# Optimization experiments

Measured on AMD Instinct MI355X. Metric: run time of the kernel, lower is better.

The kernel has to match this reference:

```python
import jax, jax.numpy as jnp
import numpy as np

B, S = 2, 1024            # 2 packed sequences, equal length (offsets = [0, 1024, 2048])
HID, H = 2560, 32
D = HID // H              # 80
ROT = int(0.4 * D)        # 32 partial rotary dims
THETA = 10000.0
MAX_POS = 2048
CACHE_SLOTS = 4096


def setup_inputs() -> dict:
    key = jax.random.key(0)
    ks = jax.random.split(key, 8)
    T = B * S
    w = lambda k: jax.random.normal(k, (HID, HID), dtype=jnp.float32) * 0.02
    return {
        "h": jax.random.normal(ks[0], (T, HID), dtype=jnp.float32),
        "k_cache": jnp.zeros((CACHE_SLOTS, HID), dtype=jnp.float32),
        "v_cache": jnp.zeros((CACHE_SLOTS, HID), dtype=jnp.float32),
        "q_w": w(ks[1]), "q_b": jnp.zeros((HID,), jnp.float32),
        "k_w": w(ks[2]), "k_b": jnp.zeros((HID,), jnp.float32),
        "v_w": w(ks[3]), "v_b": jnp.zeros((HID,), jnp.float32),
        "dense_w": w(ks[4]), "dense_b": jnp.zeros((HID,), jnp.float32),
        "positions": jnp.tile(jnp.arange(S, dtype=jnp.int32), B),
        "offsets": jnp.array([0, S, 2 * S], dtype=jnp.int32),
        "cache_indices": jnp.arange(T, dtype=jnp.int32),
    }


def _rope_tables():
    # neox-style partial rotary tables, [MAX_POS, ROT//2]
    inv_freq = 1.0 / (THETA ** (jnp.arange(0, ROT, 2, dtype=jnp.float32) / ROT))
    freqs = jnp.arange(MAX_POS, dtype=jnp.float32)[:, None] * inv_freq[None, :]
    return jnp.cos(freqs), jnp.sin(freqs)


def _apply_rope(x, cos, sin):
    # x: [T, H, D]; cos/sin: [T, ROT//2] -> rotate first ROT dims, pass rest
    c = cos[:, None, :]
    s = sin[:, None, :]
    x1, x2, rest = x[..., : ROT // 2], x[..., ROT // 2 : ROT], x[..., ROT:]
    return jnp.concatenate([x1 * c - x2 * s, x2 * c + x1 * s, rest], axis=-1)


def reference(h, k_cache, v_cache, q_w, q_b, k_w, k_b, v_w, v_b,
              dense_w, dense_b, positions, offsets, cache_indices):
    T = h.shape[0]
    q = h @ q_w + q_b
    k = h @ k_w + k_b
    v = h @ v_w + v_b

    cos_t, sin_t = _rope_tables()
    cos = cos_t[positions]
    sin = sin_t[positions]
    q = _apply_rope(q.reshape(T, H, D), cos, sin)
    k = _apply_rope(k.reshape(T, H, D), cos, sin)
    v = v.reshape(T, H, D)

    # prompt_init path: scatter freshly-rotated K/V into the flat cache
    k_cache = k_cache.at[cache_indices].set(k.reshape(T, HID))
    v_cache = v_cache.at[cache_indices].set(v.reshape(T, HID))

    # packed_attention: causal attention within each (equal-length) sequence
    q4 = q.reshape(B, S, H, D)
    k4 = k.reshape(B, S, H, D)
    v4 = v.reshape(B, S, H, D)
    scale = D ** -0.5
    scores = jnp.einsum("bqhd,bkhd->bhqk", q4, k4) * scale
    causal = jnp.tril(jnp.ones((S, S), dtype=bool))
    scores = jnp.where(causal[None, None], scores, jnp.float32(-1e9))
    p = jax.nn.softmax(scores, axis=-1)
    o = jnp.einsum("bhqk,bkhd->bqhd", p, v4).reshape(T, HID)

    return o @ dense_w + dense_b
```

## Files before the change

kernel.cpp:

```cpp
#include <hip/hip_runtime.h>
#include <hip/hip_bf16.h>

#define Bq 2
#define Sq 1024
#define Tq 2048
#define HIDq 2560
#define Hq 32
#define Dq 80
#define NQKV 7680

typedef __bf16 bf16x8 __attribute__((ext_vector_type(8)));
typedef float f32x4 __attribute__((ext_vector_type(4)));
typedef unsigned short u16x8 __attribute__((ext_vector_type(8)));
using bf16 = __hip_bfloat16;

__device__ __forceinline__ void gload_lds16(const bf16* g, bf16* l) {
  __builtin_amdgcn_global_load_lds((const __attribute__((address_space(1))) void*)g,
                                   (__attribute__((address_space(3))) void*)l,
                                   16, 0, 0);
}

__global__ __launch_bounds__(256) void cast_h_kernel(const float* __restrict__ h,
                                                     bf16* __restrict__ hb) {
  int i = (blockIdx.x * 256 + threadIdx.x) * 4;
  float4 v = *(const float4*)(h + i);
  bf16 tmp[4];
  tmp[0] = __float2bfloat16(v.x);
  tmp[1] = __float2bfloat16(v.y);
  tmp[2] = __float2bfloat16(v.z);
  tmp[3] = __float2bfloat16(v.w);
  *(ushort4*)(hb + i) = *(ushort4*)tmp;
}

__global__ __launch_bounds__(256) void bias_concat_kernel(const float* __restrict__ qb,
                                                          const float* __restrict__ kb,
                                                          const float* __restrict__ vb,
                                                          float* __restrict__ bqkv) {
  int i = blockIdx.x * 256 + threadIdx.x;
  if (i < HIDq) bqkv[i] = qb[i];
  else if (i < 2 * HIDq) bqkv[i] = kb[i - HIDq];
  else bqkv[i] = vb[i - 2 * HIDq];
}

__global__ __launch_bounds__(256) void wtrans_kernel(const float* __restrict__ qw,
                                                     const float* __restrict__ kw,
                                                     const float* __restrict__ vw,
                                                     const float* __restrict__ dw,
                                                     bf16* __restrict__ wqkvt,
                                                     bf16* __restrict__ wdt) {
  __shared__ float tile[32][33];
  const int z = blockIdx.z;
  const float* src = (z == 0) ? qw : (z == 1) ? kw : (z == 2) ? vw : dw;
  const int n0 = blockIdx.x * 32;
  const int k0 = blockIdx.y * 32;
  const int tx = threadIdx.x, ty = threadIdx.y;
#pragma unroll
  for (int r = 0; r < 4; r++)
    tile[ty + 8 * r][tx] = src[(size_t)(k0 + ty + 8 * r) * HIDq + n0 + tx];
  __syncthreads();
  bf16* dst = (z < 3) ? (wqkvt + (size_t)z * HIDq * HIDq) : wdt;
#pragma unroll
  for (int r = 0; r < 4; r++)
    dst[(size_t)(n0 + ty + 8 * r) * HIDq + k0 + tx] = __float2bfloat16(tile[tx][ty + 8 * r]);
}

__global__ __launch_bounds__(512, 2) void gemm9s_kernel(const bf16* __restrict__ A,
                                                        const bf16* __restrict__ Bt,
                                                        const float* __restrict__ bias,
                                                        bf16* __restrict__ Cout,
                                                        int N, int K, int tM) {
  __shared__ char smem[9 * 16384];
  const int tid = threadIdx.x;
  const int lane = tid & 63;
  const int ln = lane & 15, lg = lane >> 4;
  const int wave = tid >> 6;
  const int wm = wave >> 2;
  const int wn = wave & 3;

  int bid = blockIdx.x, nwg = gridDim.x, swz = bid;
  if ((nwg & 7) == 0) { int cpx = nwg >> 3; swz = (bid & 7) * cpx + (bid >> 3); }
  const int m0 = (swz % tM) * 256;
  const int n0 = (swz / tM) * 256;
  const int NT = K >> 6;

  f32x4 acc[8][4];
  const f32x4 zz = {0.f, 0.f, 0.f, 0.f};
#pragma unroll
  for (int i = 0; i < 8; ++i)
#pragma unroll
    for (int j = 0; j < 4; ++j) acc[i][j] = zz;

  int srow[2], skel[2];
#pragma unroll
  for (int c = 0; c < 2; ++c) {
    const unsigned L = (unsigned)(c * 8192 + tid * 16);
    const unsigned P = L ^ (((L >> 9) & 1u) << 5);
    srow[c] = (int)(P >> 7);
    skel[c] = (int)((P & 127u) >> 1);
  }
  const int wbase = wave * 1024;

  auto STAGE = [&](int H, int ss) {
    const int hh = H & 3;
    const int th = H >> 2;
    const bf16* mat = (hh < 2) ? A : Bt;
    const int rowbase = (hh < 2) ? (m0 + hh * 128) : (n0 + (hh - 2) * 128);
    char* dst = smem + (ss << 14);
#pragma unroll
    for (int c = 0; c < 2; ++c)
      gload_lds16(mat + (size_t)(rowbase + srow[c]) * K + th * 64 + skel[c],
                  (bf16*)(dst + c * 8192 + wbase));
  };

  unsigned offA[2][4][2];
  int     halfA[2][4];
#pragma unroll
  for (int mh = 0; mh < 2; ++mh)
#pragma unroll
    for (int i = 0; i < 4; ++i) {
      const int row = wm * 128 + mh * 64 + i * 16 + ln;
      halfA[mh][i] = row >> 7;
      const int r = row & 127;
#pragma unroll
      for (int kh = 0; kh < 2; ++kh) {
        const unsigned P = (unsigned)(r * 128 + kh * 64 + lg * 16);
        offA[mh][i][kh] = P ^ (((P >> 9) & 1u) << 5);
      }
    }
  unsigned offB[4][2];
  int     halfB[4];
#pragma unroll
  for (int j = 0; j < 4; ++j) {
    const int row = wn * 64 + j * 16 + ln;
    halfB[j] = row >> 7;
    const int r = row & 127;
#pragma unroll
    for (int kh = 0; kh < 2; ++kh) {
      const unsigned P = (unsigned)(r * 128 + kh * 64 + lg * 16);
      offB[j][kh] = P ^ (((P >> 9) & 1u) << 5);
    }
  }

#pragma unroll
  for (int H = 0; H < 5; ++H) STAGE(H, H);

  int s0 = 0;
  for (int t = 0; t < NT; ++t) {
    if (t + 1 < NT) asm volatile("s_waitcnt vmcnt(2)" ::: "memory");
    else            asm volatile("s_waitcnt vmcnt(0)" ::: "memory");
    __builtin_amdgcn_s_barrier();

    int slt[4];
#pragma unroll
    for (int h = 0; h < 4; ++h) { int s = s0 + h; if (s >= 9) s -= 9; slt[h] = s << 14; }

#pragma unroll
    for (int kh = 0; kh < 2; ++kh) {
      bf16x8 bfr[4];
#pragma unroll
      for (int j = 0; j < 4; ++j)
        bfr[j] = *(const bf16x8*)(smem + slt[2 + halfB[j]] + offB[j][kh]);
#pragma unroll
      for (int mh = 0; mh < 2; ++mh) {
        {
          const int p = kh * 2 + mh;
          const int H = 4 * t + p + 5;
          if (H < 4 * NT) {
            int s = s0 + p + 5; if (s >= 9) s -= 9;
            STAGE(H, s);
          }
        }
        bf16x8 af[4];
#pragma unroll
        for (int i = 0; i < 4; ++i)
          af[i] = *(const bf16x8*)(smem + slt[halfA[mh][i]] + offA[mh][i][kh]);
        __builtin_amdgcn_s_setprio(1);
#pragma unroll
        for (int i = 0; i < 4; ++i)
#pragma unroll
          for (int j = 0; j < 4; ++j)
            acc[mh * 4 + i][j] =
                __builtin_amdgcn_mfma_f32_16x16x32_bf16(af[i], bfr[j], acc[mh * 4 + i][j], 0, 0, 0);
        __builtin_amdgcn_s_setprio(0);
      }
    }

    s0 += 4; if (s0 >= 9) s0 -= 9;
  }

#pragma unroll
  for (int i = 0; i < 8; ++i) {
    const int rowb = m0 + wm * 128 + i * 16 + lg * 4;
#pragma unroll
    for (int r = 0; r < 4; ++r) {
#pragma unroll
      for (int j = 0; j < 4; ++j) {
        const int col = n0 + wn * 64 + j * 16 + ln;
        Cout[(size_t)(rowb + r) * N + col] = __float2bfloat16(acc[i][j][r] + bias[col]);
      }
    }
  }
}

template <int MFRAG, int NFRAG, bool OUT_BF16>
__global__ __launch_bounds__(512, 4) void gemm256_kernel(const bf16* __restrict__ A,
                                                         const bf16* __restrict__ Bt,
                                                         const float* __restrict__ bias,
                                                         void* __restrict__ Cout,
                                                         int N, int K, int tMc) {
  constexpr int ACALLS = MFRAG / 4;
  constexpr int BCALLS = NFRAG / 2;
  constexpr int APANEL = 8192 * ACALLS;
  constexpr int BUFSZ = APANEL + 8192 * BCALLS;
  __shared__ char smem[3 * BUFSZ];
  const int tid = threadIdx.x;
  const int lane = tid & 63;
  const int ln = lane & 15, lg = lane >> 4;
  const int wave = tid >> 6;
  const int wm = wave >> 2;
  const int wn = wave & 3;

  int bid = blockIdx.x;
  int swz = bid;
  int nwg = gridDim.x;
  if ((nwg & 7) == 0) { int cpx = nwg >> 3; swz = (bid & 7) * cpx + (bid >> 3); }
  const int m0 = (swz % tMc) * (32 * MFRAG);
  const int n0 = (swz / tMc) * (64 * NFRAG);

  const int NT = K >> 5;

  f32x4 acc[MFRAG][NFRAG];
  const f32x4 zz = {0.f, 0.f, 0.f, 0.f};
#pragma unroll
  for (int i = 0; i < MFRAG; ++i)
#pragma unroll
    for (int j = 0; j < NFRAG; ++j) acc[i][j] = zz;

  const int Rl0 = tid >> 2;
  const int slot = tid & 3;
  const int wbase = (tid >> 6) * 1024;

  auto STAGE = [&](int t, int b) {
    const int k0 = t << 5;
    char* Ab = smem + b * BUFSZ;
    char* Bb = Ab + APANEL;
#pragma unroll
    for (int c = 0; c < ACALLS; ++c) {
      const int srow = c * 128 + Rl0;
      const int row = srow ^ ((srow >> 2) & 1);
      const int col8 = slot ^ (row & 3);
      gload_lds16(A + (size_t)(m0 + row) * K + k0 + col8 * 8,
                  (bf16*)(Ab + c * 8192 + wbase));
    }
#pragma unroll
    for (int c = 0; c < BCALLS; ++c) {
      const int srow = c * 128 + Rl0;
      const int row = srow ^ ((srow >> 2) & 1);
      const int col8 = slot ^ (row & 3);
      gload_lds16(Bt + (size_t)(n0 + row) * K + k0 + col8 * 8,
                  (bf16*)(Bb + c * 8192 + wbase));
    }
  };

  auto FRAG = [&](const char* base, int row) -> bf16x8 {
    const unsigned off = ((unsigned)((row ^ ((row >> 2) & 1)) << 6)) |
                         (((unsigned)lg << 4) ^ ((unsigned)(row & 3) << 4));
    return *(const bf16x8*)(base + off);
  };

  auto WAIT_COUNTED = [&]() {
    constexpr int NCALLS = ACALLS + BCALLS;
    if constexpr (NCALLS == 2)      asm volatile("s_waitcnt vmcnt(2)" ::: "memory");
    else if constexpr (NCALLS == 3) asm volatile("s_waitcnt vmcnt(3)" ::: "memory");
    else                            asm volatile("s_waitcnt vmcnt(4)" ::: "memory");
  };

  STAGE(0, 0);
  STAGE(1, 1);
  WAIT_COUNTED();
  __builtin_amdgcn_s_barrier();

  for (int t = 0; t < NT; ++t) {
    const int cb = t % 3;
    const char* Ab = smem + cb * BUFSZ;
    const char* Bb = Ab + APANEL;
    if (t + 2 < NT) STAGE(t + 2, (t + 2) % 3);

    bf16x8 bfr[NFRAG];
#pragma unroll
    for (int j = 0; j < NFRAG; ++j) bfr[j] = FRAG(Bb, wn * (16 * NFRAG) + j * 16 + ln);
#pragma unroll
    for (int ph = 0; ph < ACALLS; ++ph) {
      bf16x8 af[4];
#pragma unroll
      for (int i = 0; i < 4; ++i)
        af[i] = FRAG(Ab, wm * (16 * MFRAG) + (ph * 4 + i) * 16 + ln);
      __builtin_amdgcn_s_setprio(1);
#pragma unroll
      for (int i = 0; i < 4; ++i)
#pragma unroll
        for (int j = 0; j < NFRAG; ++j)
          acc[ph * 4 + i][j] =
              __builtin_amdgcn_mfma_f32_16x16x32_bf16(af[i], bfr[j], acc[ph * 4 + i][j], 0, 0, 0);
      __builtin_amdgcn_s_setprio(0);
    }

    if (t + 2 < NT) WAIT_COUNTED();
    else            asm volatile("s_waitcnt vmcnt(0)" ::: "memory");
    __builtin_amdgcn_s_barrier();
  }

#pragma unroll
  for (int i = 0; i < MFRAG; ++i) {
    const int rowb = m0 + wm * (16 * MFRAG) + i * 16 + lg * 4;
#pragma unroll
    for (int r = 0; r < 4; ++r) {
#pragma unroll
      for (int j = 0; j < NFRAG; ++j) {
        const int col = n0 + wn * (16 * NFRAG) + j * 16 + ln;
        const float v = acc[i][j][r] + bias[col];
        if (OUT_BF16)
          ((bf16*)Cout)[(size_t)(rowb + r) * N + col] = __float2bfloat16(v);
        else
          ((float*)Cout)[(size_t)(rowb + r) * N + col] = v;
      }
    }
  }
}

__global__ __launch_bounds__(256) void rope_kernel(bf16* __restrict__ qkv,
                                                   const int* __restrict__ positions) {
  int tid = blockIdx.x * 256 + threadIdx.x;
  int i = tid & 15;
  int h = (tid >> 4) & 31;
  int t = tid >> 9;
  float pos = (float)positions[t];
  float inv = exp2f(-0.83048202372f * (float)i);
  float ang = pos * inv;
  float s, c;
  sincosf(ang, &s, &c);
  size_t base = (size_t)t * NQKV + h * Dq + i;
  {
    float x1 = __bfloat162float(qkv[base]);
    float x2 = __bfloat162float(qkv[base + 16]);
    qkv[base] = __float2bfloat16(x1 * c - x2 * s);
    qkv[base + 16] = __float2bfloat16(x2 * c + x1 * s);
  }
  base += HIDq;
  {
    float x1 = __bfloat162float(qkv[base]);
    float x2 = __bfloat162float(qkv[base + 16]);
    qkv[base] = __float2bfloat16(x1 * c - x2 * s);
    qkv[base + 16] = __float2bfloat16(x2 * c + x1 * s);
  }
}

__global__ __launch_bounds__(256) void vtrans_kernel(const bf16* __restrict__ qkv,
                                                     bf16* __restrict__ vT) {
  __shared__ bf16 tile[32][33];
  const int b = blockIdx.z;
  const int c0 = blockIdx.x * 32;
  const int s0 = blockIdx.y * 32;
  const int tx = threadIdx.x, ty = threadIdx.y;
#pragma unroll
  for (int r = 0; r < 4; r++)
    tile[ty + 8 * r][tx] = qkv[(size_t)(b * Sq + s0 + ty + 8 * r) * NQKV + 2 * HIDq + c0 + tx];
  __syncthreads();
#pragma unroll
  for (int r = 0; r < 4; r++)
    vT[(size_t)b * HIDq * Sq + (size_t)(c0 + ty + 8 * r) * Sq + s0 + tx] = tile[tx][ty + 8 * r];
}

__global__ __launch_bounds__(256) void attn_kernel(const bf16* __restrict__ qkv,
                                                   const bf16* __restrict__ vT,
                                                   bf16* __restrict__ obuf) {
  const int x = blockIdx.x;
  const int p = x >> 6;
  const int hb = x & 63;
  const int h = hb >> 1;
  const int b = hb & 1;
  __shared__ bf16 Ks[64][104];
  __shared__ bf16 Vt[80][72];
  __shared__ bf16 Ps[4][16][72];
  const int tid = threadIdx.x;
  const int wave = tid >> 6, lane = tid & 63;
  const int ln = lane & 15, lg = lane >> 4;
  const float scale = 0.1118033988749895f;
  const u16x8 zv = {0, 0, 0, 0, 0, 0, 0, 0};

#pragma unroll
  for (int qsel = 0; qsel < 2; ++qsel) {
    const int qt = qsel ? (15 - p) : p;

    bf16x8 aq[3];
    {
      const size_t qbase = (size_t)(b * Sq + qt * 64 + wave * 16 + ln) * NQKV + h * Dq;
#pragma unroll
      for (int kc = 0; kc < 3; ++kc) {
        const int col = kc * 32 + lg * 8;
        u16x8 v = zv;
        if (col < 80) v = *(const u16x8*)(qkv + qbase + col);
        aq[kc] = *(bf16x8*)&v;
      }
    }

    float mstate[4], lstate[4];
    f32x4 oacc[5];
    const f32x4 zz = {0.f, 0.f, 0.f, 0.f};
#pragma unroll
    for (int r = 0; r < 4; ++r) { mstate[r] = -__builtin_inff(); lstate[r] = 0.f; }
#pragma unroll
    for (int n = 0; n < 5; ++n) oacc[n] = zz;

    for (int j = 0; j <= qt; ++j) {
      const int kv0 = j * 64;
      __syncthreads();
      for (int idx = tid; idx < 64 * 13; idx += 256) {
        int rr = idx / 13, c8 = idx % 13;
        u16x8 val = zv;
        if (c8 < 10)
          val = *(const u16x8*)(qkv + (size_t)(b * Sq + kv0 + rr) * NQKV + HIDq + h * Dq + c8 * 8);
        *(u16x8*)&Ks[rr][c8 * 8] = val;
      }
      for (int idx = tid; idx < 80 * 8; idx += 256) {
        int rr = idx >> 3, c8 = idx & 7;
        *(u16x8*)&Vt[rr][c8 * 8] =
            *(const u16x8*)(vT + (size_t)b * HIDq * Sq + (size_t)(h * Dq + rr) * Sq + kv0 + c8 * 8);
      }
      __syncthreads();

      f32x4 sacc[4];
#pragma unroll
      for (int n = 0; n < 4; ++n) sacc[n] = zz;
#pragma unroll
      for (int kc = 0; kc < 3; ++kc) {
        bf16x8 bk[4];
#pragma unroll
        for (int n = 0; n < 4; ++n) bk[n] = *(const bf16x8*)&Ks[n * 16 + ln][kc * 32 + lg * 8];
#pragma unroll
        for (int n = 0; n < 4; ++n)
          sacc[n] = __builtin_amdgcn_mfma_f32_16x16x32_bf16(aq[kc], bk[n], sacc[n], 0, 0, 0);
      }

      const bool diag = (j == qt);
#pragma unroll
      for (int r = 0; r < 4; ++r) {
        const int qloc = wave * 16 + lg * 4 + r;
        float v[4];
        float vmax = -__builtin_inff();
#pragma unroll
        for (int n = 0; n < 4; ++n) {
          float xk = sacc[n][r] * scale;
          if (diag && (n * 16 + ln) > qloc) xk = -__builtin_inff();
          v[n] = xk;
          vmax = fmaxf(vmax, xk);
        }
#pragma unroll
        for (int off = 8; off >= 1; off >>= 1) vmax = fmaxf(vmax, __shfl_xor(vmax, off, 64));
        const float mo = mstate[r];
        const float mn = fmaxf(mo, vmax);
        const float alpha = __expf(mo - mn);
        float psum = 0.f;
#pragma unroll
        for (int n = 0; n < 4; ++n) {
          const float pv = __expf(v[n] - mn);
          psum += pv;
          Ps[wave][lg * 4 + r][n * 16 + ln] = __float2bfloat16(pv);
        }
#pragma unroll
        for (int off = 8; off >= 1; off >>= 1) psum += __shfl_xor(psum, off, 64);
        lstate[r] = lstate[r] * alpha + psum;
        mstate[r] = mn;
#pragma unroll
        for (int n5 = 0; n5 < 5; ++n5) oacc[n5][r] *= alpha;
      }
      asm volatile("s_waitcnt lgkmcnt(0)" ::: "memory");
      __builtin_amdgcn_sched_barrier(0);

#pragma unroll
      for (int kc = 0; kc < 2; ++kc) {
        bf16x8 ap = *(const bf16x8*)&Ps[wave][ln][kc * 32 + lg * 8];
        bf16x8 bv[5];
#pragma unroll
        for (int n = 0; n < 5; ++n) bv[n] = *(const bf16x8*)&Vt[n * 16 + ln][kc * 32 + lg * 8];
#pragma unroll
        for (int n = 0; n < 5; ++n)
          oacc[n] = __builtin_amdgcn_mfma_f32_16x16x32_bf16(ap, bv[n], oacc[n], 0, 0, 0);
      }
    }

#pragma unroll
    for (int r = 0; r < 4; ++r) {
      const float inv = 1.0f / lstate[r];
      const size_t rowbase =
          (size_t)(b * Sq + qt * 64 + wave * 16 + lg * 4 + r) * HIDq + h * Dq;
#pragma unroll
      for (int n5 = 0; n5 < 5; ++n5)
        obuf[rowbase + n5 * 16 + ln] = __float2bfloat16(oacc[n5][r] * inv);
    }
  }
}

extern "C" void kernel_launch(void* const* d_in, const int* in_sizes, int n_in,
                              void* d_out, int out_size, void* d_ws, size_t ws_size,
                              hipStream_t stream) {
  const float* h = (const float*)d_in[0];
  const float* q_w = (const float*)d_in[3];
  const float* q_b = (const float*)d_in[4];
  const float* k_w = (const float*)d_in[5];
  const float* k_b = (const float*)d_in[6];
  const float* v_w = (const float*)d_in[7];
  const float* v_b = (const float*)d_in[8];
  const float* dw = (const float*)d_in[9];
  const float* db = (const float*)d_in[10];
  const int* positions = (const int*)d_in[11];

  if (ws_size < 94402560ull) return;
  char* ws = (char*)d_ws;
  bf16* hb = (bf16*)(ws);
  bf16* wqkvt = (bf16*)(ws + 10485760);
  bf16* wdt = (bf16*)(ws + 49807360);
  bf16* qkv = (bf16*)(ws + 62914560);
  float* bqkv = (float*)(ws + 94371840);
  bf16* vT = hb;
  bf16* obuf = wqkvt;

  cast_h_kernel<<<5120, 256, 0, stream>>>(h, hb);
  bias_concat_kernel<<<30, 256, 0, stream>>>(q_b, k_b, v_b, bqkv);
  wtrans_kernel<<<dim3(80, 80, 4), dim3(32, 8), 0, stream>>>(q_w, k_w, v_w, dw, wqkvt, wdt);
  gemm9s_kernel<<<240, 512, 0, stream>>>(hb, wqkvt, bqkv, qkv, NQKV, HIDq, 8);
  rope_kernel<<<4096, 256, 0, stream>>>(qkv, positions);
  vtrans_kernel<<<dim3(80, 32, 2), dim3(32, 8), 0, stream>>>(qkv, vT);
  attn_kernel<<<512, 256, 0, stream>>>(qkv, vT, obuf);
  gemm256_kernel<4, 2, false><<<320, 512, 0, stream>>>(obuf, wdt, db, d_out, HIDq, HIDq, 16);
}
```

Baseline: 239.4 us.

## Restructure QKV GEMM main loop into four barrier-separated phases per K-tile

Rewrites the QKV projection GEMM's inner loop into four phases per K-step. Each phase issues its LDS fragment reads and one global-to-LDS stage, then waits on barriers before running a block of MFMAs. Each wave now maps to a single A half and a single B half, which removes the per-fragment half-slot indexing. The goal is to line up LDS reads, prefetch and MFMA across waves, ping-pong style, so the matrix units stay busy. The cost is extra barriers per K-step plus some fragment reloading, which could add stalls if the waves do not interleave well.

```diff
diff --git a/kernel.cpp b/kernel.cpp
--- a/kernel.cpp
+++ b/kernel.cpp
@@ -64,7 +64,7 @@
     dst[(size_t)(n0 + ty + 8 * r) * HIDq + k0 + tx] = __float2bfloat16(tile[tx][ty + 8 * r]);
 }
 
-__global__ __launch_bounds__(512, 2) void gemm9s_kernel(const bf16* __restrict__ A,
+__global__ __launch_bounds__(512, 2) void gemm8f_kernel(const bf16* __restrict__ A,
                                                         const bf16* __restrict__ Bt,
                                                         const float* __restrict__ bias,
                                                         bf16* __restrict__ Cout,
@@ -113,78 +113,82 @@
   };
 
   unsigned offA[2][4][2];
-  int     halfA[2][4];
 #pragma unroll
   for (int mh = 0; mh < 2; ++mh)
 #pragma unroll
     for (int i = 0; i < 4; ++i) {
-      const int row = wm * 128 + mh * 64 + i * 16 + ln;
-      halfA[mh][i] = row >> 7;
-      const int r = row & 127;
+      const int r = mh * 64 + i * 16 + ln;
 #pragma unroll
       for (int kh = 0; kh < 2; ++kh) {
         const unsigned P = (unsigned)(r * 128 + kh * 64 + lg * 16);
         offA[mh][i][kh] = P ^ (((P >> 9) & 1u) << 5);
       }
     }
-  unsigned offB[4][2];
-  int     halfB[4];
-#pragma unroll
-  for (int j = 0; j < 4; ++j) {
-    const int row = wn * 64 + j * 16 + ln;
-    halfB[j] = row >> 7;
-    const int r = row & 127;
-#pragma unroll
-    for (int kh = 0; kh < 2; ++kh) {
-      const unsigned P = (unsigned)(r * 128 + kh * 64 + lg * 16);
-      offB[j][kh] = P ^ (((P >> 9) & 1u) << 5);
-    }
-  }
+  unsigned offB[2][2][2];
+#pragma unroll
+  for (int jh = 0; jh < 2; ++jh)
+#pragma unroll
+    for (int j = 0; j < 2; ++j) {
+      const int r = (wn & 1) * 64 + (jh * 2 + j) * 16 + ln;
+#pragma unroll
+      for (int kh = 0; kh < 2; ++kh) {
+        const unsigned P = (unsigned)(r * 128 + kh * 64 + lg * 16);
+        offB[jh][j][kh] = P ^ (((P >> 9) & 1u) << 5);
+      }
+    }
 
 #pragma unroll
   for (int H = 0; H < 5; ++H) STAGE(H, H);
+  asm volatile("s_waitcnt vmcnt(2)" ::: "memory");
+  __builtin_amdgcn_s_barrier();
 
   int s0 = 0;
   for (int t = 0; t < NT; ++t) {
-    if (t + 1 < NT) asm volatile("s_waitcnt vmcnt(2)" ::: "memory");
-    else            asm volatile("s_waitcnt vmcnt(0)" ::: "memory");
-    __builtin_amdgcn_s_barrier();
-
-    int slt[4];
-#pragma unroll
-    for (int h = 0; h < 4; ++h) { int s = s0 + h; if (s >= 9) s -= 9; slt[h] = s << 14; }
-
-#pragma unroll
-    for (int kh = 0; kh < 2; ++kh) {
-      bf16x8 bfr[4];
-#pragma unroll
-      for (int j = 0; j < 4; ++j)
-        bfr[j] = *(const bf16x8*)(smem + slt[2 + halfB[j]] + offB[j][kh]);
-#pragma unroll
-      for (int mh = 0; mh < 2; ++mh) {
-        {
-          const int p = kh * 2 + mh;
-          const int H = 4 * t + p + 5;
-          if (H < 4 * NT) {
-            int s = s0 + p + 5; if (s >= 9) s -= 9;
-            STAGE(H, s);
-          }
-        }
-        bf16x8 af[4];
+    int sa = s0 + wm;             if (sa >= 9) sa -= 9;
+    int sb = s0 + 2 + (wn >> 1);  if (sb >= 9) sb -= 9;
+    const int sA = sa << 14;
+    const int sB = sb << 14;
+
+    bf16x8 af[4][2], bfr[2][2];
+#pragma unroll
+    for (int p = 0; p < 4; ++p) {
+      const int mh = p >> 1;
+      const int jh = (p == 1 || p == 2) ? 1 : 0;
+      if (p == 0 || p == 2) {
 #pragma unroll
         for (int i = 0; i < 4; ++i)
-          af[i] = *(const bf16x8*)(smem + slt[halfA[mh][i]] + offA[mh][i][kh]);
-        __builtin_amdgcn_s_setprio(1);
+#pragma unroll
+          for (int kh = 0; kh < 2; ++kh)
+            af[i][kh] = *(const bf16x8*)(smem + sA + offA[mh][i][kh]);
+      }
+      if (p != 2) {
+#pragma unroll
+        for (int j = 0; j < 2; ++j)
+#pragma unroll
+          for (int kh = 0; kh < 2; ++kh)
+            bfr[j][kh] = *(const bf16x8*)(smem + sB + offB[jh][j][kh]);
+      }
+      {
+        const int H = 4 * t + p + 5;
+        if (H < 4 * NT) { int s = s0 + p + 5; if (s >= 9) s -= 9; STAGE(H, s); }
+      }
+      __builtin_amdgcn_s_barrier();
+      asm volatile("s_waitcnt lgkmcnt(0)" ::: "memory");
+      __builtin_amdgcn_sched_barrier(0);
+      __builtin_amdgcn_s_setprio(1);
+#pragma unroll
+      for (int kh = 0; kh < 2; ++kh)
 #pragma unroll
         for (int i = 0; i < 4; ++i)
 #pragma unroll
-          for (int j = 0; j < 4; ++j)
-            acc[mh * 4 + i][j] =
-                __builtin_amdgcn_mfma_f32_16x16x32_bf16(af[i], bfr[j], acc[mh * 4 + i][j], 0, 0, 0);
-        __builtin_amdgcn_s_setprio(0);
-      }
-    }
-
+          for (int j = 0; j < 2; ++j)
+            acc[mh * 4 + i][jh * 2 + j] = __builtin_amdgcn_mfma_f32_16x16x32_bf16(
+                af[i][kh], bfr[j][kh], acc[mh * 4 + i][jh * 2 + j], 0, 0, 0);
+      __builtin_amdgcn_s_setprio(0);
+      if (p == 3 && t + 1 < NT)
+        asm volatile("s_waitcnt vmcnt(2)" ::: "memory");
+      __builtin_amdgcn_s_barrier();
+    }
     s0 += 4; if (s0 >= 9) s0 -= 9;
   }
 
@@ -528,7 +532,7 @@
   cast_h_kernel<<<5120, 256, 0, stream>>>(h, hb);
   bias_concat_kernel<<<30, 256, 0, stream>>>(q_b, k_b, v_b, bqkv);
   wtrans_kernel<<<dim3(80, 80, 4), dim3(32, 8), 0, stream>>>(q_w, k_w, v_w, dw, wqkvt, wdt);
-  gemm9s_kernel<<<240, 512, 0, stream>>>(hb, wqkvt, bqkv, qkv, NQKV, HIDq, 8);
+  gemm8f_kernel<<<240, 512, 0, stream>>>(hb, wqkvt, bqkv, qkv, NQKV, HIDq, 8);
   rope_kernel<<<4096, 256, 0, stream>>>(qkv, positions);
   vtrans_kernel<<<dim3(80, 32, 2), dim3(32, 8), 0, stream>>>(qkv, vT);
   attn_kernel<<<512, 256, 0, stream>>>(qkv, vT, obuf);
```

Result: slower. 253.7 us (+6.0%).
